# Kernel tuning notes

Measured on AMD Instinct MI355X. Metric: run time of the kernel, lower is better.

The kernel has to match this reference:

```python
import jax, jax.numpy as jnp
import numpy as np
from jax import lax

N = 50000
E = 320000
IN_DIM = 128
OUT_DIM = 64
N_CHANNEL = 8
KERNEL = 3
N_REL = 500
BN_EPS = 1e-5


def setup_inputs() -> dict:
    key = jax.random.key(0)
    ks = jax.random.split(key, 10)
    inp = jax.random.normal(ks[0], (N, IN_DIM), dtype=jnp.float32)
    heads = jax.random.randint(ks[1], (E,), 0, N)
    rels = jax.random.randint(ks[2], (E,), 0, N_REL)
    tails = jax.random.randint(ks[3], (E,), 0, N)
    triple = jnp.stack([heads, rels, tails], axis=1).astype(jnp.int64)
    # parameters
    limit_W = float(np.sqrt(6.0 / (IN_DIM + OUT_DIM)))  # xavier_uniform
    W = jax.random.uniform(ks[4], (IN_DIM, OUT_DIM), minval=-limit_W, maxval=limit_W, dtype=jnp.float32)
    rel_embed = jax.random.normal(ks[5], (N_REL, OUT_DIM), dtype=jnp.float32)
    fan_in = 1 * KERNEL * KERNEL
    b = float(1.0 / np.sqrt(fan_in))
    conv_w = jax.random.uniform(ks[6], (N_CHANNEL, 1, KERNEL, KERNEL), minval=-b, maxval=b, dtype=jnp.float32)
    conv_b = jax.random.uniform(ks[7], (N_CHANNEL,), minval=-b, maxval=b, dtype=jnp.float32)
    fc_in = N_CHANNEL * (OUT_DIM - KERNEL + 1) * (3 - KERNEL + 1)
    bf = float(1.0 / np.sqrt(fc_in))
    fc_w = jax.random.uniform(ks[8], (1, fc_in), minval=-bf, maxval=bf, dtype=jnp.float32)
    bn1_gamma = jnp.ones((1,), jnp.float32)
    bn1_beta = jnp.zeros((1,), jnp.float32)
    bn2_gamma = jnp.ones((N_CHANNEL,), jnp.float32)
    bn2_beta = jnp.zeros((N_CHANNEL,), jnp.float32)
    return {"input": inp, "triple": triple, "W": W, "rel_embed": rel_embed,
            "conv_w": conv_w, "conv_b": conv_b, "fc_w": fc_w,
            "bn1_gamma": bn1_gamma, "bn1_beta": bn1_beta,
            "bn2_gamma": bn2_gamma, "bn2_beta": bn2_beta}


def _bn_eval(x, gamma, beta):
    # eval-mode BatchNorm with running_mean=0, running_var=1
    scale = gamma / jnp.sqrt(1.0 + BN_EPS)
    return x * scale.reshape(1, -1, 1, 1) + beta.reshape(1, -1, 1, 1)


def reference(input, triple, W, rel_embed, conv_w, conv_b, fc_w,
              bn1_gamma, bn1_beta, bn2_gamma, bn2_beta):
    n = input.shape[0]
    inp = input @ W                       # [N, out_dim]
    head = triple[:, 0]
    tail = triple[:, 2]
    h = inp[head]                         # [E, D]
    r = rel_embed[triple[:, 1]]           # [E, D]
    t = inp[tail]                         # [E, D]
    # energy function: [E,1,D,3] -> bn1 -> conv -> bn2 -> relu -> fc
    x = jnp.stack([h, r, t], axis=-1)[:, None, :, :]   # [E,1,D,3]
    x = _bn_eval(x, bn1_gamma, bn1_beta)
    y = lax.conv_general_dilated(x, conv_w, (1, 1), 'VALID',
                                 dimension_numbers=('NCHW', 'OIHW', 'NCHW'))
    y = y + conv_b.reshape(1, -1, 1, 1)                 # [E,C,D-2,1]
    y = jax.nn.relu(_bn_eval(y, bn2_gamma, bn2_beta))
    y = y.reshape(y.shape[0], -1)
    e = y @ fc_w[0]                                     # [E]
    e = jax.nn.leaky_relu(e, 0.01)
    # sparse softmax over rows (head) then sparse mm with input_
    m = jax.ops.segment_max(e, head, num_segments=n)
    ex = jnp.exp(e - m[head])
    denom = jax.ops.segment_sum(ex, head, num_segments=n)
    attn = ex / denom[head]
    agg = jax.ops.segment_sum(attn[:, None] * t, head, num_segments=n)
    return jax.nn.elu(agg + inp)
```

## Files before the change

### kernel.cpp

```cpp
#include <hip/hip_runtime.h>
#include <hip/hip_bf16.h>
#include <stdint.h>

#define IN_DIM   128
#define OUT_DIM  64
#define NCH      8
#define N_REL    500
#define BN_EPS   1e-5f
#define CAP      32


__global__ __launch_bounds__(256) void k_bucket(
    const int* __restrict__ triple,
    const float* __restrict__ conv_w, const float* __restrict__ conv_b,
    const float* __restrict__ fc_w,
    const float* __restrict__ bn1g, const float* __restrict__ bn1b,
    const float* __restrict__ bn2g, const float* __restrict__ bn2b,
    const float* __restrict__ rel_embed,
    int* __restrict__ cnt, int2* __restrict__ rt32,
    float* __restrict__ cw, float* __restrict__ fcf, float* __restrict__ relf,
    int E, int N)
{
    const int tid  = blockIdx.x * blockDim.x + threadIdx.x;
    const int nthr = gridDim.x * blockDim.x;

    for (int i = tid; i < N_REL * OUT_DIM; i += nthr) relf[i] = rel_embed[i];
    for (int i = tid; i < NCH * 62;        i += nthr) fcf[i]  = fc_w[i];
    if (tid == 0) {
        float rs  = rsqrtf(1.f + BN_EPS);
        float s1  = bn1g[0] * rs;
        float be1 = bn1b[0];
        for (int c = 0; c < NCH; ++c) {
            float s2 = bn2g[c] * rs;
            float k1 = s1 * s2;
            float wsum = 0.f;
            for (int d = 0; d < 3; ++d) {
                float a  = conv_w[c * 9 + d * 3 + 0];
                float b  = conv_w[c * 9 + d * 3 + 1];
                float cc = conv_w[c * 9 + d * 3 + 2];
                wsum += a + b + cc;
                cw[c * 3 + d]      = k1 * a;
                cw[24 + c * 3 + d] = k1 * b;
                cw[48 + c * 3 + d] = k1 * cc;
            }
            cw[72 + c] = (be1 * wsum + conv_b[c]) * s2 + bn2b[c];
        }
    }

    for (int j = tid; j < E; j += nthr) {
        int h = triple[3 * j], r = triple[3 * j + 1], t = triple[3 * j + 2];
        h = min(max(h, 0), N - 1);
        r = min(max(r, 0), N_REL - 1);
        t = min(max(t, 0), N - 1);
        int pos = atomicAdd(&cnt[h], 1);
        if (pos < CAP) rt32[(unsigned)h * CAP + pos] = make_int2(r, t);
    }
}

__global__ __launch_bounds__(256) void k_gemm(
    const float* __restrict__ X, const float* __restrict__ W,
    float* __restrict__ out, int N)
{
    __shared__ float Wl[IN_DIM * OUT_DIM];
    __shared__ float Xl[32 * IN_DIM];
    const int rows0 = blockIdx.x * 32;

    const float4* W4 = (const float4*)W;
    for (int i = threadIdx.x; i < IN_DIM * OUT_DIM / 4; i += 256)
        ((float4*)Wl)[i] = W4[i];
    for (int i = threadIdx.x; i < 32 * IN_DIM / 4; i += 256) {
        int r = i >> 5, k4 = i & 31;
        int rr = rows0 + r;
        float4 v = make_float4(0.f, 0.f, 0.f, 0.f);
        if (rr < N) v = ((const float4*)X)[(unsigned)rr * (IN_DIM / 4) + k4];
        ((float4*)Xl)[i] = v;
    }
    __syncthreads();

    const int w = threadIdx.x >> 6;
    const int c = threadIdx.x & 63;
    float acc[8];
    #pragma unroll
    for (int r = 0; r < 8; ++r) acc[r] = 0.f;

    for (int k4 = 0; k4 < IN_DIM / 4; ++k4) {
        int k = k4 * 4;
        float w0 = Wl[(k + 0) * OUT_DIM + c];
        float w1 = Wl[(k + 1) * OUT_DIM + c];
        float w2 = Wl[(k + 2) * OUT_DIM + c];
        float w3 = Wl[(k + 3) * OUT_DIM + c];
        #pragma unroll
        for (int r = 0; r < 8; ++r) {
            const float4 x = *(const float4*)&Xl[(w * 8 + r) * IN_DIM + k];
            acc[r] = fmaf(x.w, w3, fmaf(x.z, w2, fmaf(x.y, w1, fmaf(x.x, w0, acc[r]))));
        }
    }
    #pragma unroll
    for (int r = 0; r < 8; ++r) {
        int rr = rows0 + w * 8 + r;
        if (rr < N) out[(unsigned)rr * OUT_DIM + c] = acc[r];
    }
}

__device__ __forceinline__ float dpp_wave_sum(float x) {
    x += __int_as_float(__builtin_amdgcn_update_dpp(0, __float_as_int(x), 0x111, 0xf, 0xf, true));
    x += __int_as_float(__builtin_amdgcn_update_dpp(0, __float_as_int(x), 0x112, 0xf, 0xf, true));
    x += __int_as_float(__builtin_amdgcn_update_dpp(0, __float_as_int(x), 0x114, 0xf, 0xf, true));
    x += __int_as_float(__builtin_amdgcn_update_dpp(0, __float_as_int(x), 0x118, 0xf, 0xf, true));
    x += __int_as_float(__builtin_amdgcn_update_dpp(0, __float_as_int(x), 0x142, 0xf, 0xf, true));
    x += __int_as_float(__builtin_amdgcn_update_dpp(0, __float_as_int(x), 0x143, 0xf, 0xf, true));
    return __int_as_float(__builtin_amdgcn_readlane(__float_as_int(x), 63));
}

__global__ __launch_bounds__(256, 4) void k_fused_all(
    const float* __restrict__ inp, const float* __restrict__ relf,
    const float* __restrict__ cw, const float* __restrict__ fcf,
    const int* __restrict__ cnt, const int2* __restrict__ rt32,
    float* __restrict__ out, int N)
{
    const int lane   = threadIdx.x & 63;
    const int wave   = (blockIdx.x * (blockDim.x >> 6)) + (threadIdx.x >> 6);
    const int nwaves = gridDim.x * (blockDim.x >> 6);

    float fcl[NCH];
    #pragma unroll
    for (int c = 0; c < NCH; ++c)
        fcl[c] = (lane < 62) ? fcf[c * 62 + lane] : 0.f;

    for (int h = wave; h < N; h += nwaves) {
        const int deg = min(cnt[h], CAP);

        float h0 = inp[(unsigned)h * OUT_DIM + lane];
        float h1 = __shfl_down(h0, 1, 64), h2 = __shfl_down(h0, 2, 64);
        float Ht[NCH];
        #pragma unroll
        for (int c = 0; c < NCH; ++c) {
            float v = cw[72 + c];
            v = fmaf(cw[c * 3 + 0], h0, v);
            v = fmaf(cw[c * 3 + 1], h1, v);
            v = fmaf(cw[c * 3 + 2], h2, v);
            Ht[c] = v;
        }

        float m_run = -INFINITY, l_run = 0.f, agg = 0.f;

        int2 rtv = make_int2(0, 0);
        if (lane < deg) rtv = rt32[(unsigned)h * CAP + lane];

        if (deg > 0) {
            int rk = __builtin_amdgcn_readlane(rtv.x, 0);
            int tk = __builtin_amdgcn_readlane(rtv.y, 0);
            float rr = relf[(unsigned)rk * OUT_DIM + lane];
            float tt = inp [(unsigned)tk * OUT_DIM + lane];

            for (int k = 0; k < deg; ++k) {
                float rrN = 0.f, ttN = 0.f;
                if (k + 1 < deg) {
                    int rk1 = __builtin_amdgcn_readlane(rtv.x, k + 1);
                    int tk1 = __builtin_amdgcn_readlane(rtv.y, k + 1);
                    rrN = relf[(unsigned)rk1 * OUT_DIM + lane];
                    ttN = inp [(unsigned)tk1 * OUT_DIM + lane];
                }
                float r1 = __shfl_down(rr, 1, 64), r2 = __shfl_down(rr, 2, 64);
                float t1 = __shfl_down(tt, 1, 64), t2 = __shfl_down(tt, 2, 64);

                float acc = 0.f;
                #pragma unroll
                for (int c = 0; c < NCH; ++c) {
                    float y = Ht[c];
                    y = fmaf(cw[24 + c * 3 + 0], rr, y);
                    y = fmaf(cw[24 + c * 3 + 1], r1, y);
                    y = fmaf(cw[24 + c * 3 + 2], r2, y);
                    y = fmaf(cw[48 + c * 3 + 0], tt, y);
                    y = fmaf(cw[48 + c * 3 + 1], t1, y);
                    y = fmaf(cw[48 + c * 3 + 2], t2, y);
                    acc = fmaf(fmaxf(y, 0.f), fcl[c], acc);
                }
                float s  = dpp_wave_sum(acc);
                float ev = fmaxf(s, 0.01f * s);

                float mn = fmaxf(m_run, ev);
                float sc = __expf(m_run - mn);
                float wk = __expf(ev - mn);
                agg   = fmaf(agg, sc, wk * tt);
                l_run = fmaf(l_run, sc, wk);
                m_run = mn;

                rr = rrN; tt = ttN;
            }
        }
        float aggn = (l_run > 0.f) ? agg / l_run : 0.f;
        float x = aggn + h0;
        float y = x > 0.f ? x : expm1f(x);
        out[(unsigned)h * OUT_DIM + lane] = y;
    }
}

extern "C" void kernel_launch(void* const* d_in, const int* in_sizes, int n_in,
                              void* d_out, int out_size, void* d_ws, size_t ws_size,
                              hipStream_t stream)
{
    const float* input     = (const float*)d_in[0];
    const int*   triple    = (const int*)d_in[1];
    const float* W         = (const float*)d_in[2];
    const float* rel_embed = (const float*)d_in[3];
    const float* conv_w    = (const float*)d_in[4];
    const float* conv_b    = (const float*)d_in[5];
    const float* fc_w      = (const float*)d_in[6];
    const float* bn1g      = (const float*)d_in[7];
    const float* bn1b      = (const float*)d_in[8];
    const float* bn2g      = (const float*)d_in[9];
    const float* bn2b      = (const float*)d_in[10];
    float*       out       = (float*)d_out;

    const int N = in_sizes[0] / IN_DIM;
    const int E = in_sizes[1] / 3;

    auto align = [](size_t x) { return (x + 255) & ~(size_t)255; };
    char* base = (char*)d_ws;
    size_t o = 0;
    float* inp   = (float*)(base + o); o = align(o + (size_t)N * OUT_DIM * 4);
    int2*  rt32  = (int2*)(base + o);  o = align(o + (size_t)N * CAP * 8);
    float* cw    = (float*)(base + o); o = align(o + 80 * 4);
    float* fcf   = (float*)(base + o); o = align(o + 496 * 4);
    float* relf  = (float*)(base + o); o = align(o + (size_t)N_REL * OUT_DIM * 4);
    size_t zero_off = o;
    int*   cnt   = (int*)(base + o);   o = align(o + (size_t)N * 4);
    size_t zero_bytes = o - zero_off;

    hipMemsetAsync(base + zero_off, 0, zero_bytes, stream);

    k_bucket<<<(E + 255) / 256, 256, 0, stream>>>(
        triple, conv_w, conv_b, fc_w, bn1g, bn1b, bn2g, bn2b, rel_embed,
        cnt, rt32, cw, fcf, relf, E, N);
    k_gemm<<<(N + 31) / 32, 256, 0, stream>>>(input, W, inp, N);
    k_fused_all<<<4096, 256, 0, stream>>>(inp, relf, cw, fcf, cnt, rt32, out, N);
}
```

Before: 198.3 us.

## Fuse GEMM and bucketing into one persistent kernel, drop parameter copies

Merges the bucketing kernel and the input-projection GEMM into a single grid-stride kernel of 1024 blocks. The GEMM now reads X and W straight from global memory instead of staging them in LDS, and the constant folding is spread over 8 threads. The copies of rel_embed and fc_w into workspace are removed, and the fused kernel reads the original inputs directly. ELU's expm1f is replaced with __expf(x)-1, which trades some precision near zero for speed. Fewer launches, but the GEMM loses LDS reuse and runs serially before bucketing inside each block.

Result: no change. 200.5 us (+1.1%).

```diff
diff --git a/kernel.cpp b/kernel.cpp
--- a/kernel.cpp
+++ b/kernel.cpp
@@ -10,95 +10,82 @@
 #define CAP      32
 
 
-__global__ __launch_bounds__(256) void k_bucket(
+__device__ __forceinline__ void fold_cw_thread(
+    const float* __restrict__ conv_w, const float* __restrict__ conv_b,
+    const float* __restrict__ bn1g, const float* __restrict__ bn1b,
+    const float* __restrict__ bn2g, const float* __restrict__ bn2b,
+    float* __restrict__ cw, int c)
+{
+    if (c >= NCH) return;
+    float rs  = rsqrtf(1.f + BN_EPS);
+    float s1  = bn1g[0] * rs;
+    float be1 = bn1b[0];
+    float s2  = bn2g[c] * rs;
+    float k1  = s1 * s2;
+    float wsum = 0.f;
+    for (int d = 0; d < 3; ++d) {
+        float a  = conv_w[c * 9 + d * 3 + 0];
+        float b  = conv_w[c * 9 + d * 3 + 1];
+        float cc = conv_w[c * 9 + d * 3 + 2];
+        wsum += a + b + cc;
+        cw[c * 3 + d]      = k1 * a;
+        cw[24 + c * 3 + d] = k1 * b;
+        cw[48 + c * 3 + d] = k1 * cc;
+    }
+    cw[72 + c] = (be1 * wsum + conv_b[c]) * s2 + bn2b[c];
+}
+
+__global__ __launch_bounds__(256) void k_build(
+    const float* __restrict__ X, const float* __restrict__ W,
     const int* __restrict__ triple,
     const float* __restrict__ conv_w, const float* __restrict__ conv_b,
-    const float* __restrict__ fc_w,
     const float* __restrict__ bn1g, const float* __restrict__ bn1b,
     const float* __restrict__ bn2g, const float* __restrict__ bn2b,
-    const float* __restrict__ rel_embed,
-    int* __restrict__ cnt, int2* __restrict__ rt32,
-    float* __restrict__ cw, float* __restrict__ fcf, float* __restrict__ relf,
-    int E, int N)
-{
-    const int tid  = blockIdx.x * blockDim.x + threadIdx.x;
-    const int nthr = gridDim.x * blockDim.x;
-
-    for (int i = tid; i < N_REL * OUT_DIM; i += nthr) relf[i] = rel_embed[i];
-    for (int i = tid; i < NCH * 62;        i += nthr) fcf[i]  = fc_w[i];
-    if (tid == 0) {
-        float rs  = rsqrtf(1.f + BN_EPS);
-        float s1  = bn1g[0] * rs;
-        float be1 = bn1b[0];
-        for (int c = 0; c < NCH; ++c) {
-            float s2 = bn2g[c] * rs;
-            float k1 = s1 * s2;
-            float wsum = 0.f;
-            for (int d = 0; d < 3; ++d) {
-                float a  = conv_w[c * 9 + d * 3 + 0];
-                float b  = conv_w[c * 9 + d * 3 + 1];
-                float cc = conv_w[c * 9 + d * 3 + 2];
-                wsum += a + b + cc;
-                cw[c * 3 + d]      = k1 * a;
-                cw[24 + c * 3 + d] = k1 * b;
-                cw[48 + c * 3 + d] = k1 * cc;
+    float* __restrict__ inp, int* __restrict__ cnt, int2* __restrict__ rt32,
+    float* __restrict__ cw, int E, int N)
+{
+    const int gtid    = blockIdx.x * 256 + threadIdx.x;
+    const int gstride = gridDim.x * 256;
+
+    if (blockIdx.x == 0 && threadIdx.x < NCH)
+        fold_cw_thread(conv_w, conv_b, bn1g, bn1b, bn2g, bn2b, cw, threadIdx.x);
+
+    const int wv = __builtin_amdgcn_readfirstlane(threadIdx.x >> 6);
+    const int ln = threadIdx.x & 63;
+    const int ntiles = (N + 31) / 32;
+    for (int tile = blockIdx.x; tile < ntiles; tile += gridDim.x) {
+        const int rows0 = tile * 32 + wv * 8;
+        float acc[8];
+        #pragma unroll
+        for (int r = 0; r < 8; ++r) acc[r] = 0.f;
+        #pragma unroll 2
+        for (int k4 = 0; k4 < IN_DIM / 4; ++k4) {
+            const int k = k4 * 4;
+            float w0 = W[(k + 0) * OUT_DIM + ln];
+            float w1 = W[(k + 1) * OUT_DIM + ln];
+            float w2 = W[(k + 2) * OUT_DIM + ln];
+            float w3 = W[(k + 3) * OUT_DIM + ln];
+            #pragma unroll
+            for (int r = 0; r < 8; ++r) {
+                const int row = min(rows0 + r, N - 1);
+                const float4 x = *(const float4*)(X + (unsigned)row * IN_DIM + k);
+                acc[r] = fmaf(x.w, w3, fmaf(x.z, w2, fmaf(x.y, w1, fmaf(x.x, w0, acc[r]))));
             }
-            cw[72 + c] = (be1 * wsum + conv_b[c]) * s2 + bn2b[c];
-        }
-    }
-
-    for (int j = tid; j < E; j += nthr) {
+        }
+        #pragma unroll
+        for (int r = 0; r < 8; ++r) {
+            const int row = rows0 + r;
+            if (row < N) inp[(unsigned)row * OUT_DIM + ln] = acc[r];
+        }
+    }
+
+    for (int j = gtid; j < E; j += gstride) {
         int h = triple[3 * j], r = triple[3 * j + 1], t = triple[3 * j + 2];
         h = min(max(h, 0), N - 1);
         r = min(max(r, 0), N_REL - 1);
         t = min(max(t, 0), N - 1);
         int pos = atomicAdd(&cnt[h], 1);
         if (pos < CAP) rt32[(unsigned)h * CAP + pos] = make_int2(r, t);
-    }
-}
-
-__global__ __launch_bounds__(256) void k_gemm(
-    const float* __restrict__ X, const float* __restrict__ W,
-    float* __restrict__ out, int N)
-{
-    __shared__ float Wl[IN_DIM * OUT_DIM];
-    __shared__ float Xl[32 * IN_DIM];
-    const int rows0 = blockIdx.x * 32;
-
-    const float4* W4 = (const float4*)W;
-    for (int i = threadIdx.x; i < IN_DIM * OUT_DIM / 4; i += 256)
-        ((float4*)Wl)[i] = W4[i];
-    for (int i = threadIdx.x; i < 32 * IN_DIM / 4; i += 256) {
-        int r = i >> 5, k4 = i & 31;
-        int rr = rows0 + r;
-        float4 v = make_float4(0.f, 0.f, 0.f, 0.f);
-        if (rr < N) v = ((const float4*)X)[(unsigned)rr * (IN_DIM / 4) + k4];
-        ((float4*)Xl)[i] = v;
-    }
-    __syncthreads();
-
-    const int w = threadIdx.x >> 6;
-    const int c = threadIdx.x & 63;
-    float acc[8];
-    #pragma unroll
-    for (int r = 0; r < 8; ++r) acc[r] = 0.f;
-
-    for (int k4 = 0; k4 < IN_DIM / 4; ++k4) {
-        int k = k4 * 4;
-        float w0 = Wl[(k + 0) * OUT_DIM + c];
-        float w1 = Wl[(k + 1) * OUT_DIM + c];
-        float w2 = Wl[(k + 2) * OUT_DIM + c];
-        float w3 = Wl[(k + 3) * OUT_DIM + c];
-        #pragma unroll
-        for (int r = 0; r < 8; ++r) {
-            const float4 x = *(const float4*)&Xl[(w * 8 + r) * IN_DIM + k];
-            acc[r] = fmaf(x.w, w3, fmaf(x.z, w2, fmaf(x.y, w1, fmaf(x.x, w0, acc[r]))));
-        }
-    }
-    #pragma unroll
-    for (int r = 0; r < 8; ++r) {
-        int rr = rows0 + w * 8 + r;
-        if (rr < N) out[(unsigned)rr * OUT_DIM + c] = acc[r];
     }
 }
 
@@ -113,8 +100,8 @@
 }
 
 __global__ __launch_bounds__(256, 4) void k_fused_all(
-    const float* __restrict__ inp, const float* __restrict__ relf,
-    const float* __restrict__ cw, const float* __restrict__ fcf,
+    const float* __restrict__ inp, const float* __restrict__ rel_embed,
+    const float* __restrict__ cw, const float* __restrict__ fc_w,
     const int* __restrict__ cnt, const int2* __restrict__ rt32,
     float* __restrict__ out, int N)
 {
@@ -125,7 +112,7 @@
     float fcl[NCH];
     #pragma unroll
     for (int c = 0; c < NCH; ++c)
-        fcl[c] = (lane < 62) ? fcf[c * 62 + lane] : 0.f;
+        fcl[c] = (lane < 62) ? fc_w[c * 62 + lane] : 0.f;
 
     for (int h = wave; h < N; h += nwaves) {
         const int deg = min(cnt[h], CAP);
@@ -143,23 +130,22 @@
         }
 
         float m_run = -INFINITY, l_run = 0.f, agg = 0.f;
-
         int2 rtv = make_int2(0, 0);
         if (lane < deg) rtv = rt32[(unsigned)h * CAP + lane];
 
         if (deg > 0) {
             int rk = __builtin_amdgcn_readlane(rtv.x, 0);
             int tk = __builtin_amdgcn_readlane(rtv.y, 0);
-            float rr = relf[(unsigned)rk * OUT_DIM + lane];
-            float tt = inp [(unsigned)tk * OUT_DIM + lane];
+            float rr = rel_embed[(unsigned)rk * OUT_DIM + lane];
+            float tt = inp      [(unsigned)tk * OUT_DIM + lane];
 
             for (int k = 0; k < deg; ++k) {
                 float rrN = 0.f, ttN = 0.f;
                 if (k + 1 < deg) {
                     int rk1 = __builtin_amdgcn_readlane(rtv.x, k + 1);
                     int tk1 = __builtin_amdgcn_readlane(rtv.y, k + 1);
-                    rrN = relf[(unsigned)rk1 * OUT_DIM + lane];
-                    ttN = inp [(unsigned)tk1 * OUT_DIM + lane];
+                    rrN = rel_embed[(unsigned)rk1 * OUT_DIM + lane];
+                    ttN = inp      [(unsigned)tk1 * OUT_DIM + lane];
                 }
                 float r1 = __shfl_down(rr, 1, 64), r2 = __shfl_down(rr, 2, 64);
                 float t1 = __shfl_down(tt, 1, 64), t2 = __shfl_down(tt, 2, 64);
@@ -191,7 +177,7 @@
         }
         float aggn = (l_run > 0.f) ? agg / l_run : 0.f;
         float x = aggn + h0;
-        float y = x > 0.f ? x : expm1f(x);
+        float y = x > 0.f ? x : (__expf(x) - 1.f);
         out[(unsigned)h * OUT_DIM + lane] = y;
     }
 }
@@ -219,20 +205,16 @@
     auto align = [](size_t x) { return (x + 255) & ~(size_t)255; };
     char* base = (char*)d_ws;
     size_t o = 0;
-    float* inp   = (float*)(base + o); o = align(o + (size_t)N * OUT_DIM * 4);
-    int2*  rt32  = (int2*)(base + o);  o = align(o + (size_t)N * CAP * 8);
-    float* cw    = (float*)(base + o); o = align(o + 80 * 4);
-    float* fcf   = (float*)(base + o); o = align(o + 496 * 4);
-    float* relf  = (float*)(base + o); o = align(o + (size_t)N_REL * OUT_DIM * 4);
-    size_t zero_off = o;
-    int*   cnt   = (int*)(base + o);   o = align(o + (size_t)N * 4);
-    size_t zero_bytes = o - zero_off;
-
-    hipMemsetAsync(base + zero_off, 0, zero_bytes, stream);
-
-    k_bucket<<<(E + 255) / 256, 256, 0, stream>>>(
-        triple, conv_w, conv_b, fc_w, bn1g, bn1b, bn2g, bn2b, rel_embed,
-        cnt, rt32, cw, fcf, relf, E, N);
-    k_gemm<<<(N + 31) / 32, 256, 0, stream>>>(input, W, inp, N);
-    k_fused_all<<<4096, 256, 0, stream>>>(inp, relf, cw, fcf, cnt, rt32, out, N);
-}
+    float* inp  = (float*)(base + o); o = align(o + (size_t)N * OUT_DIM * 4);
+    int2*  rt32 = (int2*)(base + o);  o = align(o + (size_t)N * CAP * 8);
+    float* cw   = (float*)(base + o); o = align(o + 80 * 4);
+    int*   cnt  = (int*)(base + o);   o = align(o + (size_t)N * 4);
+
+    hipMemsetAsync(cnt, 0, (size_t)N * 4, stream);
+
+    k_build<<<1024, 256, 0, stream>>>(
+        input, W, triple, conv_w, conv_b, bn1g, bn1b, bn2g, bn2b,
+        inp, cnt, rt32, cw, E, N);
+    k_fused_all<<<4096, 256, 0, stream>>>(inp, rel_embed, cw, fc_w,
+                                          cnt, rt32, out, N);
+}
```
